# Kernel optimization log

Measured on AMD Instinct MI355X. Metric: run time of the kernel, lower is better.

Reference implementation:

```python
import jax, jax.numpy as jnp
import numpy as np
from functools import partial

EPSILON = 0.1
NUM_ITERS = 100
STAB = 1e-8


def _sq_cdist(x1, x2):
    # squared euclidean distances, matching torch.cdist(p=2)**2
    s1 = jnp.sum(x1 * x1, axis=1)  # [n1]
    s2 = jnp.sum(x2 * x2, axis=1)  # [n2]
    d = s1[:, None] + s2[None, :] - 2.0 * (x1 @ x2.T)
    return jnp.maximum(d, 0.0)


def _transport_cost(x1, x2):
    n1, n2 = x1.shape[0], x2.shape[0]
    mu = jnp.full((n1,), 1.0 / n1, dtype=x1.dtype)
    nu = jnp.full((n2,), 1.0 / n2, dtype=x2.dtype)
    cost = _sq_cdist(x1, x2)          # [n1, n2]
    kernel = jnp.exp(-cost / EPSILON)  # [n1, n2]

    def body(carry, _):
        u, v = carry
        v = nu / (kernel.T @ u + STAB)
        u = mu / (kernel @ v + STAB)
        return (u, v), None

    (u, v), _ = jax.lax.scan(body, (jnp.ones_like(mu), jnp.ones_like(nu)), None, length=NUM_ITERS)
    plan = u[:, None] * kernel * v[None, :]
    return jnp.sum(plan * cost)


def setup_inputs() -> dict:
    key = jax.random.key(0)
    k1, k2 = jax.random.split(key)
    # scale 0.25 keeps squared distances O(0.3) so exp(-d/0.1) stays in range
    source = 0.25 * jax.random.uniform(k1, (8192, 32), dtype=jnp.float32)
    target = 0.25 * jax.random.uniform(k2, (8192, 32), dtype=jnp.float32)
    return {"source": source, "target": target}


def reference(source, target):
    n = source.shape[0]
    w_st = _transport_cost(source, target)
    w_ss = _transport_cost(source, source)
    w_tt = _transport_cost(target, target)
    cost = w_st - 0.5 * w_ss - 0.5 * w_tt  # debiased Sinkhorn divergence
    return cost / n  # reduction='mean'
```

## Files before the change

### kernel.cpp

```cpp
#include <hip/hip_runtime.h>

#define NN 8192
#define DD 32
#define SIDX(c) ((c) + 4 * ((c) >> 4))

constexpr float kEps   = 0.1f;
constexpr float kStab  = 1e-8f;
constexpr float kMass  = 1.0f / 8192.0f;
constexpr float kInvSc = 1.0f / 256.0f;
constexpr float kLnSc  = 5.545177444479562f;

typedef float v2f __attribute__((ext_vector_type(2)));

__device__ inline void cvt8x4(unsigned int w, float* out) {
    v2f lo = __builtin_amdgcn_cvt_pk_f32_fp8(w, false);
    v2f hi = __builtin_amdgcn_cvt_pk_f32_fp8(w, true);
    out[0] = lo.x; out[1] = lo.y; out[2] = hi.x; out[3] = hi.y;
}
__device__ inline void cvt16(uint4 kk, float* f) {
    cvt8x4(kk.x, f); cvt8x4(kk.y, f + 4); cvt8x4(kk.z, f + 8); cvt8x4(kk.w, f + 12);
}
__device__ inline void cvt16v2(uint4 kk, v2f* f) {
    f[0] = __builtin_amdgcn_cvt_pk_f32_fp8(kk.x, false);
    f[1] = __builtin_amdgcn_cvt_pk_f32_fp8(kk.x, true);
    f[2] = __builtin_amdgcn_cvt_pk_f32_fp8(kk.y, false);
    f[3] = __builtin_amdgcn_cvt_pk_f32_fp8(kk.y, true);
    f[4] = __builtin_amdgcn_cvt_pk_f32_fp8(kk.z, false);
    f[5] = __builtin_amdgcn_cvt_pk_f32_fp8(kk.z, true);
    f[6] = __builtin_amdgcn_cvt_pk_f32_fp8(kk.w, false);
    f[7] = __builtin_amdgcn_cvt_pk_f32_fp8(kk.w, true);
}
__device__ inline unsigned int pack8x4(float a, float b, float c, float d) {
    int v = 0;
    v = __builtin_amdgcn_cvt_pk_fp8_f32(a, b, v, false);
    v = __builtin_amdgcn_cvt_pk_fp8_f32(c, d, v, true);
    return (unsigned int)v;
}
__device__ inline unsigned int bf16pk(float a, float b) {
    unsigned int ua = __float_as_uint(a), ub = __float_as_uint(b);
    ua = (ua + 0x7FFFu + ((ua >> 16) & 1u)) >> 16;
    ub = (ub + 0x7FFFu + ((ub >> 16) & 1u)) >> 16;
    return ua | (ub << 16);
}
__device__ inline float dot16p(uint4 kk, const v2f* vv) {
    v2f f[8];
    cvt16v2(kk, f);
    v2f acc = {0.f, 0.f};
#pragma unroll
    for (int i = 0; i < 8; i++) acc = __builtin_elementwise_fma(f[i], vv[i], acc);
    return acc.x + acc.y;
}
__device__ inline void axpy16p(uint4 kk, float ur, v2f* ca) {
    v2f f[8];
    cvt16v2(kk, f);
    const v2f u2 = {ur, ur};
#pragma unroll
    for (int i = 0; i < 8; i++) ca[i] = __builtin_elementwise_fma(f[i], u2, ca[i]);
}
__device__ inline float wsum16(uint4 kk, const v2f* vv, const float* glut) {
    float a = 0.f;
    const unsigned int wd[4] = {kk.x, kk.y, kk.z, kk.w};
#pragma unroll
    for (int j = 0; j < 4; j++) {
        const unsigned int wv = wd[j];
        a = fmaf(vv[2 * j].x,     glut[wv & 255u], a);
        a = fmaf(vv[2 * j].y,     glut[(wv >> 8) & 255u], a);
        a = fmaf(vv[2 * j + 1].x, glut[(wv >> 16) & 255u], a);
        a = fmaf(vv[2 * j + 1].y, glut[wv >> 24], a);
    }
    return a;
}

__global__ void sk_init_u(float* __restrict__ u) {
    u[blockIdx.x * 256 + threadIdx.x] = 1.0f;
}

__global__ __launch_bounds__(256) void sk_build_k(const float* __restrict__ X,
                                                  const float* __restrict__ Y,
                                                  unsigned char* __restrict__ K) {
    __shared__ float xs[DD * 160];
    __shared__ float ys[DD * 160];
    __shared__ float sx[128], sy[128];
    const int t  = threadIdx.x;
    const int r0 = blockIdx.y * 128, c0 = blockIdx.x * 128;

    for (int idx = t; idx < DD * 128; idx += 256) {
        int d = idx >> 7, row = idx & 127;
        xs[d * 160 + SIDX(row)] = X[(size_t)(r0 + row) * DD + d];
        ys[d * 160 + SIDX(row)] = Y[(size_t)(c0 + row) * DD + d];
    }
    __syncthreads();
    if (t < 128) {
        const int si = SIDX(t);
        float s = 0.f;
        for (int d = 0; d < DD; d++) { float v = xs[d * 160 + si]; s = fmaf(v, v, s); }
        sx[t] = s;
    } else {
        const int q = t - 128, si = SIDX(q);
        float s = 0.f;
        for (int d = 0; d < DD; d++) { float v = ys[d * 160 + si]; s = fmaf(v, v, s); }
        sy[q] = s;
    }
    __syncthreads();

    const int tr = t >> 4, tc = t & 15;
    const int xb = SIDX(8 * tr);
    const int yb = SIDX(8 * tc);
    float acc[8][8] = {};
#pragma unroll 4
    for (int d = 0; d < DD; d++) {
        const float* xrow = &xs[d * 160];
        const float* yrow = &ys[d * 160];
        const float4 xa0 = *reinterpret_cast<const float4*>(&xrow[xb]);
        const float4 xa1 = *reinterpret_cast<const float4*>(&xrow[xb + 4]);
        const float4 yb0 = *reinterpret_cast<const float4*>(&yrow[yb]);
        const float4 yb1 = *reinterpret_cast<const float4*>(&yrow[yb + 4]);
        const float xv[8] = {xa0.x, xa0.y, xa0.z, xa0.w, xa1.x, xa1.y, xa1.z, xa1.w};
        const float yv[8] = {yb0.x, yb0.y, yb0.z, yb0.w, yb1.x, yb1.y, yb1.z, yb1.w};
#pragma unroll
        for (int a = 0; a < 8; a++)
#pragma unroll
            for (int b = 0; b < 8; b++) acc[a][b] = fmaf(xv[a], yv[b], acc[a][b]);
    }
#pragma unroll
    for (int a = 0; a < 8; a++) {
        const int r = r0 + 8 * tr + a;
        const float sxa = sx[8 * tr + a];
        float e[8];
#pragma unroll
        for (int b = 0; b < 8; b++) {
            float cost = sxa + sy[8 * tc + b] - 2.0f * acc[a][b];
            cost = fmaxf(cost, 0.0f);
            e[b] = __expf(fmaf(-10.0f, cost, kLnSc));
        }
        uint2 pk;
        pk.x = pack8x4(e[0], e[1], e[2], e[3]);
        pk.y = pack8x4(e[4], e[5], e[6], e[7]);
        *reinterpret_cast<uint2*>(&K[(size_t)r * NN + c0 + 8 * tc]) = pk;
    }
}

__global__ __launch_bounds__(256) void sk_colsum(const unsigned char* __restrict__ K8,
                                                 const float* __restrict__ u,
                                                 float* __restrict__ rc_out) {
    __shared__ float us[128];
    __shared__ float red[4 * 1280];
    const int t = threadIdx.x, lane = t & 63, w = t >> 6;
    const int z = blockIdx.z;
    const int c0 = blockIdx.x * 1024, r0 = blockIdx.y * 128;
    const unsigned char* K = K8 + (size_t)z * NN * NN;
    if (t < 128) us[t] = u[z * NN + r0 + t];
    __syncthreads();

    float acc[16] = {};
    const unsigned char* p = K + (size_t)(r0 + 32 * w) * NN + c0 + 16 * lane;
    for (int i = 0; i < 32; i += 4) {
        uint4 k0 = *reinterpret_cast<const uint4*>(p);
        uint4 k1 = *reinterpret_cast<const uint4*>(p + (size_t)NN);
        uint4 k2 = *reinterpret_cast<const uint4*>(p + (size_t)2 * NN);
        uint4 k3 = *reinterpret_cast<const uint4*>(p + (size_t)3 * NN);
        p += (size_t)4 * NN;
        const float u0 = us[32 * w + i + 0], u1 = us[32 * w + i + 1];
        const float u2 = us[32 * w + i + 2], u3 = us[32 * w + i + 3];
        float f[16];
        cvt16(k0, f);
#pragma unroll
        for (int j = 0; j < 16; j++) acc[j] = fmaf(f[j], u0, acc[j]);
        cvt16(k1, f);
#pragma unroll
        for (int j = 0; j < 16; j++) acc[j] = fmaf(f[j], u1, acc[j]);
        cvt16(k2, f);
#pragma unroll
        for (int j = 0; j < 16; j++) acc[j] = fmaf(f[j], u2, acc[j]);
        cvt16(k3, f);
#pragma unroll
        for (int j = 0; j < 16; j++) acc[j] = fmaf(f[j], u3, acc[j]);
    }
    float* rw = &red[w * 1280 + 20 * lane];
#pragma unroll
    for (int g = 0; g < 4; g++) {
        float4 v = {acc[4 * g + 0], acc[4 * g + 1], acc[4 * g + 2], acc[4 * g + 3]};
        *reinterpret_cast<float4*>(rw + 4 * g) = v;
    }
    __syncthreads();
    for (int c = t; c < 1024; c += 256) {
        const int sc = SIDX(c);
        const float s = red[sc] + red[1280 + sc] + red[2560 + sc] + red[3840 + sc];
        atomicAdd(&rc_out[z * NN + c0 + c], s);
    }
}

__global__ void sk_v(const float* __restrict__ rc, float* __restrict__ v) {
    const int i = (blockIdx.z * gridDim.x + blockIdx.x) * 256 + threadIdx.x;
    v[i] = kMass * __builtin_amdgcn_rcpf(fmaf(rc[i], kInvSc, kStab));
}

__global__ __launch_bounds__(512, 2) void sk_iter(const unsigned char* __restrict__ K8,
                                                  const float* __restrict__ v_in,
                                                  unsigned short* __restrict__ rcp,
                                                  float* __restrict__ u_out,
                                                  double* __restrict__ wacc,
                                                  int last) {
    __shared__ float cs[10240];
    __shared__ float red[8][8][4];
    __shared__ float glut[256];
    __shared__ double wred[8];
    const int t = threadIdx.x, lane = t & 63, w = t >> 6;
    const int z = blockIdx.z;
    const unsigned char* K = K8 + (size_t)z * NN * NN;
    const int rowbase = blockIdx.x * 32;
    const int c0 = 1024 * w;

    if (last && t < 256) {
        v2f d = __builtin_amdgcn_cvt_pk_f32_fp8((unsigned int)t, false);
        const float f = d.x;
        glut[t] = (f > 0.f) ? f * __logf(f * kInvSc) : 0.f;
    }

    v2f vv[8];
    {
        const float* vz = v_in + (size_t)z * NN + c0 + 16 * lane;
        const float4 q0 = reinterpret_cast<const float4*>(vz)[0];
        const float4 q1 = reinterpret_cast<const float4*>(vz)[1];
        const float4 q2 = reinterpret_cast<const float4*>(vz)[2];
        const float4 q3 = reinterpret_cast<const float4*>(vz)[3];
        vv[0] = {q0.x, q0.y}; vv[1] = {q0.z, q0.w};
        vv[2] = {q1.x, q1.y}; vv[3] = {q1.z, q1.w};
        vv[4] = {q2.x, q2.y}; vv[5] = {q2.z, q2.w};
        vv[6] = {q3.x, q3.y}; vv[7] = {q3.z, q3.w};
    }

    const unsigned char* kp = K + (size_t)rowbase * NN + c0 + 16 * lane;
    uint4 n0 = *reinterpret_cast<const uint4*>(kp);
    uint4 n1 = *reinterpret_cast<const uint4*>(kp + (size_t)NN);
    uint4 n2 = *reinterpret_cast<const uint4*>(kp + (size_t)2 * NN);
    uint4 n3 = *reinterpret_cast<const uint4*>(kp + (size_t)3 * NN);

    v2f ca[8] = {{0,0},{0,0},{0,0},{0,0},{0,0},{0,0},{0,0},{0,0}};
    double dacc = 0.0;
#pragma unroll 1
    for (int g = 0; g < 8; g++) {
        const uint4 k0 = n0, k1 = n1, k2 = n2, k3 = n3;
        if (g < 7) {
            const unsigned char* np = kp + (size_t)(4 * (g + 1)) * NN;
            n0 = *reinterpret_cast<const uint4*>(np);
            n1 = *reinterpret_cast<const uint4*>(np + (size_t)NN);
            n2 = *reinterpret_cast<const uint4*>(np + (size_t)2 * NN);
            n3 = *reinterpret_cast<const uint4*>(np + (size_t)3 * NN);
        }
        float p0 = dot16p(k0, vv);
        float p1 = dot16p(k1, vv);
        float p2 = dot16p(k2, vv);
        float p3 = dot16p(k3, vv);
#pragma unroll
        for (int off = 32; off > 0; off >>= 1) {
            p0 += __shfl_down(p0, off);
            p1 += __shfl_down(p1, off);
            p2 += __shfl_down(p2, off);
            p3 += __shfl_down(p3, off);
        }
        if (lane == 0) {
            red[g][w][0] = p0; red[g][w][1] = p1;
            red[g][w][2] = p2; red[g][w][3] = p3;
        }
        __syncthreads();
        float ug[4];
#pragma unroll
        for (int r = 0; r < 4; r++) {
            float s = 0.f;
#pragma unroll
            for (int ww = 0; ww < 8; ww++) s += red[g][ww][r];
            ug[r] = kMass / (s * kInvSc + kStab);
            if (w == 0 && lane == r) u_out[(size_t)z * NN + rowbase + 4 * g + r] = ug[r];
        }
        if (!last) {
            axpy16p(k0, ug[0], ca);
            axpy16p(k1, ug[1], ca);
            axpy16p(k2, ug[2], ca);
            axpy16p(k3, ug[3], ca);
        } else {
            dacc += (double)ug[0] * (double)wsum16(k0, vv, glut);
            dacc += (double)ug[1] * (double)wsum16(k1, vv, glut);
            dacc += (double)ug[2] * (double)wsum16(k2, vv, glut);
            dacc += (double)ug[3] * (double)wsum16(k3, vv, glut);
        }
    }
    if (last) {
        for (int off = 32; off > 0; off >>= 1) dacc += __shfl_down(dacc, off);
        if (lane == 0) wred[w] = dacc;
        __syncthreads();
        if (t == 0) {
            double tot = 0.0;
#pragma unroll
            for (int i = 0; i < 8; i++) tot += wred[i];
            atomicAdd(&wacc[z], -(double)kEps * (double)kInvSc * tot);
        }
        return;
    }

    {
        float* b0 = &cs[SIDX(c0 + 16 * lane)];
        float4 o0 = {ca[0].x, ca[0].y, ca[1].x, ca[1].y};
        float4 o1 = {ca[2].x, ca[2].y, ca[3].x, ca[3].y};
        float4 o2 = {ca[4].x, ca[4].y, ca[5].x, ca[5].y};
        float4 o3 = {ca[6].x, ca[6].y, ca[7].x, ca[7].y};
        *reinterpret_cast<float4*>(b0 + 0)  = o0;
        *reinterpret_cast<float4*>(b0 + 4)  = o1;
        *reinterpret_cast<float4*>(b0 + 8)  = o2;
        *reinterpret_cast<float4*>(b0 + 12) = o3;
    }
    __syncthreads();
    unsigned short* rp = rcp + ((size_t)z * 256 + blockIdx.x) * NN;
    for (int i = 8 * t; i < NN; i += 4096) {
        const int base = SIDX(i);
        float4 fa = *reinterpret_cast<const float4*>(&cs[base]);
        float4 fb = *reinterpret_cast<const float4*>(&cs[base + 4]);
        uint4 o;
        o.x = bf16pk(fa.x, fa.y); o.y = bf16pk(fa.z, fa.w);
        o.z = bf16pk(fb.x, fb.y); o.w = bf16pk(fb.z, fb.w);
        *reinterpret_cast<uint4*>(&rp[i]) = o;
    }
}

__global__ __launch_bounds__(256) void sk_reduce(const unsigned short* __restrict__ rcp,
                                                 float* __restrict__ v_out) {
    __shared__ float red[32 * 64];
    const int t = threadIdx.x, g = t & 7, q = t >> 3;
    const int z = blockIdx.z;
    const int c0 = blockIdx.x * 64;
    const unsigned short* base = rcp + (size_t)z * 256 * NN + c0 + 8 * g;
    float acc[8] = {};
#pragma unroll
    for (int r = 0; r < 8; r++) {
        uint4 hv = *reinterpret_cast<const uint4*>(base + (size_t)(8 * q + r) * NN);
        const unsigned int h[4] = {hv.x, hv.y, hv.z, hv.w};
#pragma unroll
        for (int j = 0; j < 4; j++) {
            acc[2 * j]     += __uint_as_float((h[j] & 0xFFFFu) << 16);
            acc[2 * j + 1] += __uint_as_float(h[j] & 0xFFFF0000u);
        }
    }
    float* rw = &red[q * 64 + g * 8];
    *reinterpret_cast<float4*>(rw)     = {acc[0], acc[1], acc[2], acc[3]};
    *reinterpret_cast<float4*>(rw + 4) = {acc[4], acc[5], acc[6], acc[7]};
    __syncthreads();
    if (t < 64) {
        float s = 0.f;
#pragma unroll 8
        for (int q2 = 0; q2 < 32; q2++) s += red[q2 * 64 + t];
        v_out[(size_t)z * NN + c0 + t] =
            kMass * __builtin_amdgcn_rcpf(fmaf(s, kInvSc, kStab));
    }
}

__global__ void sk_combine(const double* __restrict__ acc, float* __restrict__ out) {
    if (threadIdx.x == 0)
        out[0] = (float)((acc[0] - 0.5 * acc[1] - 0.5 * acc[2]) / 8192.0);
}

extern "C" void kernel_launch(void* const* d_in, const int* in_sizes, int n_in,
                              void* d_out, int out_size, void* d_ws, size_t ws_size,
                              hipStream_t stream) {
    const float* src = (const float*)d_in[0];
    const float* tgt = (const float*)d_in[1];
    float* out = (float*)d_out;
    char* ws = (char*)d_ws;

    const size_t need3 = 3ull * NN * NN + 3ull * 256 * NN * 2 + 16ull * NN * 4 + 1024;
    const bool batched = ws_size >= need3;
    const int B = batched ? 3 : 1;

    unsigned char*  K8  = (unsigned char*)ws;
    unsigned short* rcp = (unsigned short*)(ws + (size_t)B * NN * NN);
    float*  vb   = (float*)((char*)rcp + (size_t)B * 256 * NN * 2);
    float*  u    = vb + (size_t)B * NN;
    float*  rc0  = u + (size_t)B * NN;
    double* wacc = (double*)(rc0 + (size_t)B * NN);

    hipMemsetAsync(wacc, 0, 3 * sizeof(double), stream);
    const float* pts[3][2] = {{src, tgt}, {src, src}, {tgt, tgt}};

    if (batched) {
        hipMemsetAsync(rc0, 0, 3ull * NN * sizeof(float), stream);
        sk_init_u<<<3 * NN / 256, 256, 0, stream>>>(u);
        for (int i = 0; i < 3; i++)
            sk_build_k<<<dim3(64, 64, 1), 256, 0, stream>>>(pts[i][0], pts[i][1],
                                                            K8 + (size_t)i * NN * NN);
        sk_colsum<<<dim3(8, 64, 3), 256, 0, stream>>>(K8, u, rc0);
        sk_v<<<dim3(32, 1, 3), 256, 0, stream>>>(rc0, vb);
        for (int t = 1; t <= 100; t++) {
            sk_iter<<<dim3(256, 1, 3), 512, 0, stream>>>(K8, vb, rcp, u, wacc,
                                                         t == 100 ? 1 : 0);
            if (t < 100)
                sk_reduce<<<dim3(128, 1, 3), 256, 0, stream>>>(rcp, vb);
        }
    } else {
        for (int tf = 0; tf < 3; tf++) {
            hipMemsetAsync(rc0, 0, 1ull * NN * sizeof(float), stream);
            sk_init_u<<<NN / 256, 256, 0, stream>>>(u);
            sk_build_k<<<dim3(64, 64, 1), 256, 0, stream>>>(pts[tf][0], pts[tf][1], K8);
            sk_colsum<<<dim3(8, 64, 1), 256, 0, stream>>>(K8, u, rc0);
            sk_v<<<dim3(32, 1, 1), 256, 0, stream>>>(rc0, vb);
            for (int t = 1; t <= 100; t++) {
                sk_iter<<<dim3(256, 1, 1), 512, 0, stream>>>(K8, vb, rcp, u, &wacc[tf],
                                                             t == 100 ? 1 : 0);
                if (t < 100)
                    sk_reduce<<<dim3(128, 1, 1), 256, 0, stream>>>(rcp, vb);
            }
        }
    }
    sk_combine<<<1, 64, 0, stream>>>(wacc, out);
}
```

Baseline: 4.915 ms.

## Fuse initial column sums into K build and drop LDS staging in sk_iter

The first column-sum pass, with u all ones, is computed inside sk_build_k from the unquantized exp values through a shared-memory reduction and atomics. This removes the separate sk_colsum kernel and the sk_init_u kernel, and the three build launches become a single z-batched launch. sk_iter no longer writes u or stages its partial column sums through a large LDS buffer; each lane writes its bf16 partials straight to global memory. The LDS cut may raise occupancy, but the direct per-lane stores may coalesce less well, and the initial column sums now come from fp32 values rather than the fp8-quantized K.

```diff
diff --git a/kernel.cpp b/kernel.cpp
--- a/kernel.cpp
+++ b/kernel.cpp
@@ -16,9 +16,6 @@
     v2f lo = __builtin_amdgcn_cvt_pk_f32_fp8(w, false);
     v2f hi = __builtin_amdgcn_cvt_pk_f32_fp8(w, true);
     out[0] = lo.x; out[1] = lo.y; out[2] = hi.x; out[3] = hi.y;
-}
-__device__ inline void cvt16(uint4 kk, float* f) {
-    cvt8x4(kk.x, f); cvt8x4(kk.y, f + 4); cvt8x4(kk.z, f + 8); cvt8x4(kk.w, f + 12);
 }
 __device__ inline void cvt16v2(uint4 kk, v2f* f) {
     f[0] = __builtin_amdgcn_cvt_pk_f32_fp8(kk.x, false);
@@ -71,16 +68,20 @@
     return a;
 }
 
-__global__ void sk_init_u(float* __restrict__ u) {
-    u[blockIdx.x * 256 + threadIdx.x] = 1.0f;
-}
-
-__global__ __launch_bounds__(256) void sk_build_k(const float* __restrict__ X,
-                                                  const float* __restrict__ Y,
-                                                  unsigned char* __restrict__ K) {
+__global__ __launch_bounds__(256) void sk_build_k(const float* __restrict__ src,
+                                                  const float* __restrict__ tgt,
+                                                  unsigned char* __restrict__ K8,
+                                                  float* __restrict__ rc,
+                                                  int nb) {
     __shared__ float xs[DD * 160];
     __shared__ float ys[DD * 160];
     __shared__ float sx[128], sy[128];
+    const int z = blockIdx.z;
+    const float* X = src; const float* Y = tgt;
+    if (nb == 3) { if (z == 1) Y = src; else if (z == 2) X = tgt; }
+    unsigned char* K = K8 + (size_t)z * NN * NN;
+    float* rcz = rc + (size_t)z * NN;
+
     const int t  = threadIdx.x;
     const int r0 = blockIdx.y * 128, c0 = blockIdx.x * 128;
 
@@ -122,6 +123,7 @@
 #pragma unroll
             for (int b = 0; b < 8; b++) acc[a][b] = fmaf(xv[a], yv[b], acc[a][b]);
     }
+    float colacc[8] = {};
 #pragma unroll
     for (int a = 0; a < 8; a++) {
         const int r = r0 + 8 * tr + a;
@@ -132,61 +134,23 @@
             float cost = sxa + sy[8 * tc + b] - 2.0f * acc[a][b];
             cost = fmaxf(cost, 0.0f);
             e[b] = __expf(fmaf(-10.0f, cost, kLnSc));
+            colacc[b] += e[b];
         }
         uint2 pk;
         pk.x = pack8x4(e[0], e[1], e[2], e[3]);
         pk.y = pack8x4(e[4], e[5], e[6], e[7]);
         *reinterpret_cast<uint2*>(&K[(size_t)r * NN + c0 + 8 * tc]) = pk;
     }
-}
-
-__global__ __launch_bounds__(256) void sk_colsum(const unsigned char* __restrict__ K8,
-                                                 const float* __restrict__ u,
-                                                 float* __restrict__ rc_out) {
-    __shared__ float us[128];
-    __shared__ float red[4 * 1280];
-    const int t = threadIdx.x, lane = t & 63, w = t >> 6;
-    const int z = blockIdx.z;
-    const int c0 = blockIdx.x * 1024, r0 = blockIdx.y * 128;
-    const unsigned char* K = K8 + (size_t)z * NN * NN;
-    if (t < 128) us[t] = u[z * NN + r0 + t];
-    __syncthreads();
-
-    float acc[16] = {};
-    const unsigned char* p = K + (size_t)(r0 + 32 * w) * NN + c0 + 16 * lane;
-    for (int i = 0; i < 32; i += 4) {
-        uint4 k0 = *reinterpret_cast<const uint4*>(p);
-        uint4 k1 = *reinterpret_cast<const uint4*>(p + (size_t)NN);
-        uint4 k2 = *reinterpret_cast<const uint4*>(p + (size_t)2 * NN);
-        uint4 k3 = *reinterpret_cast<const uint4*>(p + (size_t)3 * NN);
-        p += (size_t)4 * NN;
-        const float u0 = us[32 * w + i + 0], u1 = us[32 * w + i + 1];
-        const float u2 = us[32 * w + i + 2], u3 = us[32 * w + i + 3];
-        float f[16];
-        cvt16(k0, f);
-#pragma unroll
-        for (int j = 0; j < 16; j++) acc[j] = fmaf(f[j], u0, acc[j]);
-        cvt16(k1, f);
-#pragma unroll
-        for (int j = 0; j < 16; j++) acc[j] = fmaf(f[j], u1, acc[j]);
-        cvt16(k2, f);
-#pragma unroll
-        for (int j = 0; j < 16; j++) acc[j] = fmaf(f[j], u2, acc[j]);
-        cvt16(k3, f);
-#pragma unroll
-        for (int j = 0; j < 16; j++) acc[j] = fmaf(f[j], u3, acc[j]);
-    }
-    float* rw = &red[w * 1280 + 20 * lane];
-#pragma unroll
-    for (int g = 0; g < 4; g++) {
-        float4 v = {acc[4 * g + 0], acc[4 * g + 1], acc[4 * g + 2], acc[4 * g + 3]};
-        *reinterpret_cast<float4*>(rw + 4 * g) = v;
-    }
-    __syncthreads();
-    for (int c = t; c < 1024; c += 256) {
-        const int sc = SIDX(c);
-        const float s = red[sc] + red[1280 + sc] + red[2560 + sc] + red[3840 + sc];
-        atomicAdd(&rc_out[z * NN + c0 + c], s);
+    __syncthreads();
+    float* colred = xs;
+#pragma unroll
+    for (int b = 0; b < 8; b++) colred[tr * 128 + 8 * tc + b] = colacc[b];
+    __syncthreads();
+    if (t < 128) {
+        float s = 0.f;
+#pragma unroll
+        for (int q = 0; q < 16; q++) s += colred[q * 128 + t];
+        atomicAdd(&rcz[c0 + t], s);
     }
 }
 
@@ -198,10 +162,8 @@
 __global__ __launch_bounds__(512, 2) void sk_iter(const unsigned char* __restrict__ K8,
                                                   const float* __restrict__ v_in,
                                                   unsigned short* __restrict__ rcp,
-                                                  float* __restrict__ u_out,
                                                   double* __restrict__ wacc,
                                                   int last) {
-    __shared__ float cs[10240];
     __shared__ float red[8][8][4];
     __shared__ float glut[256];
     __shared__ double wred[8];
@@ -271,7 +233,6 @@
 #pragma unroll
             for (int ww = 0; ww < 8; ww++) s += red[g][ww][r];
             ug[r] = kMass / (s * kInvSc + kStab);
-            if (w == 0 && lane == r) u_out[(size_t)z * NN + rowbase + 4 * g + r] = ug[r];
         }
         if (!last) {
             axpy16p(k0, ug[0], ca);
@@ -298,28 +259,14 @@
         return;
     }
 
-    {
-        float* b0 = &cs[SIDX(c0 + 16 * lane)];
-        float4 o0 = {ca[0].x, ca[0].y, ca[1].x, ca[1].y};
-        float4 o1 = {ca[2].x, ca[2].y, ca[3].x, ca[3].y};
-        float4 o2 = {ca[4].x, ca[4].y, ca[5].x, ca[5].y};
-        float4 o3 = {ca[6].x, ca[6].y, ca[7].x, ca[7].y};
-        *reinterpret_cast<float4*>(b0 + 0)  = o0;
-        *reinterpret_cast<float4*>(b0 + 4)  = o1;
-        *reinterpret_cast<float4*>(b0 + 8)  = o2;
-        *reinterpret_cast<float4*>(b0 + 12) = o3;
-    }
-    __syncthreads();
-    unsigned short* rp = rcp + ((size_t)z * 256 + blockIdx.x) * NN;
-    for (int i = 8 * t; i < NN; i += 4096) {
-        const int base = SIDX(i);
-        float4 fa = *reinterpret_cast<const float4*>(&cs[base]);
-        float4 fb = *reinterpret_cast<const float4*>(&cs[base + 4]);
-        uint4 o;
-        o.x = bf16pk(fa.x, fa.y); o.y = bf16pk(fa.z, fa.w);
-        o.z = bf16pk(fb.x, fb.y); o.w = bf16pk(fb.z, fb.w);
-        *reinterpret_cast<uint4*>(&rp[i]) = o;
-    }
+    unsigned short* rp = rcp + ((size_t)z * 256 + blockIdx.x) * NN + c0 + 16 * lane;
+    uint4 o0, o1;
+    o0.x = bf16pk(ca[0].x, ca[0].y); o0.y = bf16pk(ca[1].x, ca[1].y);
+    o0.z = bf16pk(ca[2].x, ca[2].y); o0.w = bf16pk(ca[3].x, ca[3].y);
+    o1.x = bf16pk(ca[4].x, ca[4].y); o1.y = bf16pk(ca[5].x, ca[5].y);
+    o1.z = bf16pk(ca[6].x, ca[6].y); o1.w = bf16pk(ca[7].x, ca[7].y);
+    *reinterpret_cast<uint4*>(rp)     = o0;
+    *reinterpret_cast<uint4*>(rp + 8) = o1;
 }
 
 __global__ __launch_bounds__(256) void sk_reduce(const unsigned short* __restrict__ rcp,
@@ -366,43 +313,37 @@
     float* out = (float*)d_out;
     char* ws = (char*)d_ws;
 
-    const size_t need3 = 3ull * NN * NN + 3ull * 256 * NN * 2 + 16ull * NN * 4 + 1024;
+    const size_t need3 = 3ull * NN * NN + 3ull * 256 * NN * 2 + 8ull * NN * 4 + 1024;
     const bool batched = ws_size >= need3;
     const int B = batched ? 3 : 1;
 
     unsigned char*  K8  = (unsigned char*)ws;
     unsigned short* rcp = (unsigned short*)(ws + (size_t)B * NN * NN);
     float*  vb   = (float*)((char*)rcp + (size_t)B * 256 * NN * 2);
-    float*  u    = vb + (size_t)B * NN;
-    float*  rc0  = u + (size_t)B * NN;
+    float*  rc0  = vb + (size_t)B * NN;
     double* wacc = (double*)(rc0 + (size_t)B * NN);
 
     hipMemsetAsync(wacc, 0, 3 * sizeof(double), stream);
-    const float* pts[3][2] = {{src, tgt}, {src, src}, {tgt, tgt}};
 
     if (batched) {
         hipMemsetAsync(rc0, 0, 3ull * NN * sizeof(float), stream);
-        sk_init_u<<<3 * NN / 256, 256, 0, stream>>>(u);
-        for (int i = 0; i < 3; i++)
-            sk_build_k<<<dim3(64, 64, 1), 256, 0, stream>>>(pts[i][0], pts[i][1],
-                                                            K8 + (size_t)i * NN * NN);
-        sk_colsum<<<dim3(8, 64, 3), 256, 0, stream>>>(K8, u, rc0);
+        sk_build_k<<<dim3(64, 64, 3), 256, 0, stream>>>(src, tgt, K8, rc0, 3);
         sk_v<<<dim3(32, 1, 3), 256, 0, stream>>>(rc0, vb);
         for (int t = 1; t <= 100; t++) {
-            sk_iter<<<dim3(256, 1, 3), 512, 0, stream>>>(K8, vb, rcp, u, wacc,
+            sk_iter<<<dim3(256, 1, 3), 512, 0, stream>>>(K8, vb, rcp, wacc,
                                                          t == 100 ? 1 : 0);
             if (t < 100)
                 sk_reduce<<<dim3(128, 1, 3), 256, 0, stream>>>(rcp, vb);
         }
     } else {
+        const float* pts[3][2] = {{src, tgt}, {src, src}, {tgt, tgt}};
         for (int tf = 0; tf < 3; tf++) {
             hipMemsetAsync(rc0, 0, 1ull * NN * sizeof(float), stream);
-            sk_init_u<<<NN / 256, 256, 0, stream>>>(u);
-            sk_build_k<<<dim3(64, 64, 1), 256, 0, stream>>>(pts[tf][0], pts[tf][1], K8);
-            sk_colsum<<<dim3(8, 64, 1), 256, 0, stream>>>(K8, u, rc0);
+            sk_build_k<<<dim3(64, 64, 1), 256, 0, stream>>>(pts[tf][0], pts[tf][1],
+                                                            K8, rc0, 1);
             sk_v<<<dim3(32, 1, 1), 256, 0, stream>>>(rc0, vb);
             for (int t = 1; t <= 100; t++) {
-                sk_iter<<<dim3(256, 1, 1), 512, 0, stream>>>(K8, vb, rcp, u, &wacc[tf],
+                sk_iter<<<dim3(256, 1, 1), 512, 0, stream>>>(K8, vb, rcp, &wacc[tf],
                                                              t == 100 ? 1 : 0);
                 if (t < 100)
                     sk_reduce<<<dim3(128, 1, 1), 256, 0, stream>>>(rcp, vb);
```

Measured after the change: 4.651 ms. -5.4%, faster.
